# Kernel tuning notes

Measured on AMD Instinct MI355X. Metric: run time of the kernel, lower is better.

Reference implementation:

```python
import jax, jax.numpy as jnp
import numpy as np

_D4H = (np.array([
    0,0,0,0, -4,0,0,0, -2,-2,-2,-2, -2,-2,-2,0, -2,-2,-2,2, -2,-2,0,-2, -2,-2,0,0, -2,-2,0,2,
    -2,-2,2,-2, -2,-2,2,0, -2,-2,2,2, -2,0,-2,-2, -2,0,-2,0, -2,0,-2,2, -2,0,0,-2, -2,0,0,0,
    -2,0,0,2, -2,0,2,-2, -2,0,2,0, -2,0,2,2, -2,2,-2,-2, -2,2,-2,0, -2,2,-2,2, -2,2,0,-2,
    -2,2,0,0, -2,2,0,2, -2,2,2,-2, -2,2,2,0, -2,2,2,2, 0,-4,0,0, 0,-2,-2,-2, 0,-2,-2,0,
    0,-2,-2,2, 0,-2,0,-2, 0,-2,0,0, 0,-2,0,2, 0,-2,2,-2, 0,-2,2,0, 0,-2,2,2, 0,0,-4,0,
    0,0,-2,-2, 0,0,-2,0, 0,0,-2,2, 0,0,0,-4, 0,0,0,-2,
    -3,-1,-3,-1, -3,-1,-3,1, -3,-1,-1,-3, -3,-1,-1,-1, -3,-1,-1,1, -3,-1,-1,3, -3,-1,1,-3, -3,-1,1,-1,
    -3,-1,1,1, -3,-1,1,3, -3,-1,3,-1, -3,-1,3,1, -3,1,-3,-1, -3,1,-3,1, -3,1,-1,-3, -3,1,-1,-1,
    -3,1,-1,1, -3,1,-1,3, -3,1,1,-3, -3,1,1,-1, -3,1,1,1, -3,1,1,3, -3,1,3,-1, -3,1,3,1,
    -3,3,-1,-1, -3,3,1,-1, -3,3,1,1, -1,-3,-3,-1, -1,-3,-3,1, -1,-3,-1,-3, -1,-3,-1,-1, -1,-3,-1,1,
    -1,-3,-1,3, -1,-3,1,-3, -1,-3,1,-1, -1,-3,1,1, -1,-3,1,3, -1,-3,3,-1, -1,-3,3,1, -1,-1,-3,-3,
    -1,-1,-3,-1, -1,-1,-3,1, -1,-1,-3,3, -1,-1,-1,-3, -1,-1,-1,-1, -1,-1,-1,1, -1,-1,-1,3, -1,-1,1,-3,
    -1,-1,1,-1, -1,-1,1,1, -1,-1,1,3, -1,-1,3,-3, -1,-1,3,-1, -1,-1,3,1, -1,-1,3,3, -1,1,-3,-3,
    -1,1,-3,-1, -1,1,-3,1, -1,1,-3,3, -1,1,-1,-3, -1,1,-1,-1, -1,1,-1,1, -1,1,-1,3, -1,1,1,-3,
    -1,1,1,-1, -1,1,1,1, -1,1,1,3, -1,1,3,-3, -1,1,3,-1, -1,1,3,1, -1,1,3,3, -1,3,-3,-1,
    -1,3,-3,1, -1,3,-1,-3, -1,3,-1,-1, -1,3,-1,1, -1,3,-1,3, -1,3,1,-3, -1,3,1,-1, -1,3,1,1,
    -1,3,1,3, -1,3,3,-1, -1,3,3,1
], dtype=np.float32).reshape(128, 4) / 2.0)

M_OUT = 4096   # out_features (q1*q2)
IN_F = 4096    # in_features (p1*p2)
NGRP = IN_F // 4
BATCH = 256

def setup_inputs():
    key = jax.random.key(0)
    k1, k2, k3, k4 = jax.random.split(key, 4)
    return {
        "input": jax.random.normal(k1, (BATCH, IN_F), jnp.float32),
        "scaleW_DSC": jax.random.uniform(k2, (IN_F,), jnp.float32, 0.5, 1.5),
        "Qscales": jax.random.uniform(k3, (NGRP,), jnp.float32, 0.5, 1.5),
        "Qidxs": jax.random.randint(k4, (M_OUT, NGRP), 0, 256, jnp.int32),
    }

def reference(input, scaleW_DSC, Qscales, Qidxs):
    D4H = jnp.asarray(_D4H)
    # incoherence / diagonal scaling of activations, then per-group-of-4 quant scales
    x = (input.reshape(-1, IN_F) * scaleW_DSC).reshape(-1, NGRP, 4)  # [b, n, 4]
    x = x * Qscales[None, :, None]
    # dequantize weights from the D4 half-codebook: top bit = sign, low 7 bits = row
    sign = jnp.where(Qidxs < 128, 1.0, -1.0).astype(x.dtype)         # [m, n]
    W = D4H[Qidxs & 127] * sign[:, :, None]                          # [m, n, 4]
    # z[b, i] = sum_j <x[b, j, :], W[i, j, :]>  (the indexsum8 gather-accumulate)
    z = jnp.einsum('bjk,ijk->bi', x, W)                              # [b, m]
    return z.reshape(*input.shape[:-1], M_OUT)
```

## Files before the change

kernel.cpp:

```cpp
#include <hip/hip_runtime.h>

#define DI __device__ __forceinline__

constexpr int BATCH = 256;
constexpr int INF   = 4096;
constexpr int NGRP  = 1024;
constexpr int MOUT  = 4096;

using bf16x8 = __attribute__((ext_vector_type(8))) short;
using f32x4  = __attribute__((ext_vector_type(4))) float;

__device__ __constant__ signed char D4_I8[512] = {
     0, 0, 0, 0,  -4, 0, 0, 0,  -2,-2,-2,-2,  -2,-2,-2, 0,  -2,-2,-2, 2,  -2,-2, 0,-2,  -2,-2, 0, 0,  -2,-2, 0, 2,
    -2,-2, 2,-2,  -2,-2, 2, 0,  -2,-2, 2, 2,  -2, 0,-2,-2,  -2, 0,-2, 0,  -2, 0,-2, 2,  -2, 0, 0,-2,  -2, 0, 0, 0,
    -2, 0, 0, 2,  -2, 0, 2,-2,  -2, 0, 2, 0,  -2, 0, 2, 2,  -2, 2,-2,-2,  -2, 2,-2, 0,  -2, 2,-2, 2,  -2, 2, 0,-2,
    -2, 2, 0, 0,  -2, 2, 0, 2,  -2, 2, 2,-2,  -2, 2, 2, 0,  -2, 2, 2, 2,   0,-4, 0, 0,   0,-2,-2,-2,   0,-2,-2, 0,
     0,-2,-2, 2,   0,-2, 0,-2,   0,-2, 0, 0,   0,-2, 0, 2,   0,-2, 2,-2,   0,-2, 2, 0,   0,-2, 2, 2,   0, 0,-4, 0,
     0, 0,-2,-2,   0, 0,-2, 0,   0, 0,-2, 2,   0, 0, 0,-4,   0, 0, 0,-2,
    -3,-1,-3,-1,  -3,-1,-3, 1,  -3,-1,-1,-3,  -3,-1,-1,-1,  -3,-1,-1, 1,  -3,-1,-1, 3,  -3,-1, 1,-3,  -3,-1, 1,-1,
    -3,-1, 1, 1,  -3,-1, 1, 3,  -3,-1, 3,-1,  -3,-1, 3, 1,  -3, 1,-3,-1,  -3, 1,-3, 1,  -3, 1,-1,-3,  -3, 1,-1,-1,
    -3, 1,-1, 1,  -3, 1,-1, 3,  -3, 1, 1,-3,  -3, 1, 1,-1,  -3, 1, 1, 1,  -3, 1, 1, 3,  -3, 1, 3,-1,  -3, 1, 3, 1,
    -3, 3,-1,-1,  -3, 3, 1,-1,  -3, 3, 1, 1,  -1,-3,-3,-1,  -1,-3,-3, 1,  -1,-3,-1,-3,  -1,-3,-1,-1,  -1,-3,-1, 1,
    -1,-3,-1, 3,  -1,-3, 1,-3,  -1,-3, 1,-1,  -1,-3, 1, 1,  -1,-3, 1, 3,  -1,-3, 3,-1,  -1,-3, 3, 1,  -1,-1,-3,-3,
    -1,-1,-3,-1,  -1,-1,-3, 1,  -1,-1,-3, 3,  -1,-1,-1,-3,  -1,-1,-1,-1,  -1,-1,-1, 1,  -1,-1,-1, 3,  -1,-1, 1,-3,
    -1,-1, 1,-1,  -1,-1, 1, 1,  -1,-1, 1, 3,  -1,-1, 3,-3,  -1,-1, 3,-1,  -1,-1, 3, 1,  -1,-1, 3, 3,  -1, 1,-3,-3,
    -1, 1,-3,-1,  -1, 1,-3, 1,  -1, 1,-3, 3,  -1, 1,-1,-3,  -1, 1,-1,-1,  -1, 1,-1, 1,  -1, 1,-1, 3,  -1, 1, 1,-3,
    -1, 1, 1,-1,  -1, 1, 1, 1,  -1, 1, 1, 3,  -1, 1, 3,-3,  -1, 1, 3,-1,  -1, 1, 3, 1,  -1, 1, 3, 3,  -1, 3,-3,-1,
    -1, 3,-3, 1,  -1, 3,-1,-3,  -1, 3,-1,-1,  -1, 3,-1, 1,  -1, 3,-1, 3,  -1, 3, 1,-3,  -1, 3, 1,-1,  -1, 3, 1, 1,
    -1, 3, 1, 3,  -1, 3, 3,-1,  -1, 3, 3, 1
};

DI unsigned short f2bf(float f) {
  unsigned int u = __float_as_uint(f);
  u += 0x7fffu + ((u >> 16) & 1u);
  return (unsigned short)(u >> 16);
}

__global__ __launch_bounds__(256) void prep_kernel(
    const float* __restrict__ inp, const float* __restrict__ sw,
    const float* __restrict__ qs, const int* __restrict__ qidx,
    unsigned short* __restrict__ xa, unsigned short* __restrict__ qp) {
  __shared__ unsigned short lw[16384];
  const int t = threadIdx.x;

  if (blockIdx.x < 512) {
    int i  = blockIdx.x * 256 + t;
    int j  = i & 3;
    int m  = (i >> 2) & 255;
    int kb = i >> 10;
    const float* ip = inp + (size_t)m * INF + kb * 32 + j * 8;
    float4 f0 = *reinterpret_cast<const float4*>(ip);
    float4 f1 = *reinterpret_cast<const float4*>(ip + 4);
    const float* sp = sw + kb * 32 + j * 8;
    float4 s0 = *reinterpret_cast<const float4*>(sp);
    float4 s1 = *reinterpret_cast<const float4*>(sp + 4);
    int g = kb * 8 + j * 2;
    float q0 = qs[g], q1 = qs[g + 1];
    union { unsigned short u[8]; uint4 v; } o;
    o.u[0] = f2bf(f0.x * s0.x * q0); o.u[1] = f2bf(f0.y * s0.y * q0);
    o.u[2] = f2bf(f0.z * s0.z * q0); o.u[3] = f2bf(f0.w * s0.w * q0);
    o.u[4] = f2bf(f1.x * s1.x * q1); o.u[5] = f2bf(f1.y * s1.y * q1);
    o.u[6] = f2bf(f1.z * s1.z * q1); o.u[7] = f2bf(f1.w * s1.w * q1);
    reinterpret_cast<uint4*>(xa)[i] = o.v;
    return;
  }

  const int n0 = (blockIdx.x - 512) * 32;
  char* lwb = reinterpret_cast<char*>(lw);
  const int b4w   = t >> 1;
  const int cbase = b4w * 256 + ((2 * t) & 3) * 2;
  const int xk    = (b4w & 31) << 3;
  for (int r = 0; r < 32; ++r) {
    int4 v = *reinterpret_cast<const int4*>(
        qidx + (size_t)(n0 + r) * NGRP + t * 4);
    unsigned p01 = (v.x & 255) | ((v.y & 255) << 8) |
                   ((v.z & 255) << 16) | ((unsigned)(v.w & 255) << 24);
    *reinterpret_cast<unsigned*>(lwb + cbase + ((r * 8) ^ xk)) = p01;
  }
  __syncthreads();
  for (int it = 0; it < 16; ++it) {
    int b4 = it * 8 + (t >> 5);
    int n  = t & 31;
    unsigned long long v = *reinterpret_cast<const unsigned long long*>(
        lwb + b4 * 256 + ((n * 8) ^ ((b4 & 31) << 3)));
    *reinterpret_cast<unsigned long long*>(
        reinterpret_cast<char*>(qp) + (size_t)b4 * 32768 +
        (size_t)(n0 + n) * 8) = v;
  }
}


#define MM(A, B, C) C = __builtin_amdgcn_mfma_f32_16x16x32_bf16(A, B, C, 0, 0, 0)
#define LD8(p) (*reinterpret_cast<const bf16x8*>(p))

#define BAR() do { \
    asm volatile("s_waitcnt lgkmcnt(0)\n\ts_barrier" ::: "memory"); \
    __builtin_amdgcn_sched_barrier(0); } while (0)

#define STG(QV, BUF) do { \
    ulonglong2 w_; \
    w_.x = tbl[(QV) & 255]; w_.y = tbl[(QV) >> 8]; \
    *reinterpret_cast<ulonglong2*>(wsm + wbase + (BUF) + wslot) = w_; } while (0)

#define AL(AB, T) do { \
    AB##_0 = LD8(axb + (size_t)(T) * 32768 +     0); \
    AB##_1 = LD8(axb + (size_t)(T) * 32768 +  1024); \
    AB##_2 = LD8(axb + (size_t)(T) * 32768 + 16384); \
    AB##_3 = LD8(axb + (size_t)(T) * 32768 + 17408); } while (0)

#define CMP(AB, BUFOFF) do { \
    const char* wp_ = wsm + kqW + (BUFOFF); \
    bf16x8 b00 = LD8(wp_ + rb00); \
    bf16x8 b01 = LD8(wp_ + rb00 + 2048); \
    bf16x8 b10 = LD8(wp_ + rb10); \
    bf16x8 b11 = LD8(wp_ + rb10 + 2048); \
    MM(AB##_0, b00, c00); MM(AB##_0, b01, c01); \
    MM(AB##_1, b00, c10); MM(AB##_1, b01, c11); \
    MM(AB##_2, b10, c00); MM(AB##_2, b11, c01); \
    MM(AB##_3, b10, c10); MM(AB##_3, b11, c11); } while (0)

#define STEPA(T, QN) do { \
    AL(AO, (T) + 1); STG(QN, (((T) + 1) & 1) * 4096); \
    CMP(AE, ((T) & 1) * 4096); BAR(); } while (0)
#define STEPB(T, QN) do { \
    AL(AE, (T) + 1); STG(QN, (((T) + 1) & 1) * 4096); \
    CMP(AO, ((T) & 1) * 4096); BAR(); } while (0)

__global__ __launch_bounds__(1024, 4) void gemm_kernel(
    const unsigned short* __restrict__ xa, const unsigned short* __restrict__ qp,
    float* __restrict__ out) {
  __shared__ unsigned long long tbl[256];
  __shared__ float red[12][1152];
  char* wsm = reinterpret_cast<char*>(red);

  const int tid  = threadIdx.x;
  const int lane = tid & 63;
  const int wave = tid >> 6;
  const int mh   = wave >> 2;
  const int kq   = wave & 3;
  const int l15  = lane & 15, l4 = lane >> 4;

  const int bid = blockIdx.x;
  const int ns  = bid & 127;
  const int mt  = bid >> 7;
  const int n0  = ns * 32;
  const int m0  = mt * 128 + mh * 32;

  const int kqs = tid >> 8;
  const int qn  = (tid & 255) >> 3;
  const int j2  = tid & 7;
  const unsigned wbase = (unsigned)(kqs * 8192);
  const unsigned wslot =
      ((unsigned)(qn * 128 + j2 * 16)) ^ ((unsigned)(qn & 7) << 4);

  const char* qpb = reinterpret_cast<const char*>(qp) +
      (size_t)(kqs * 32 + (j2 >> 2)) * 32768 + (size_t)(n0 + qn) * 8 +
      (j2 & 3) * 2;
#define QLD(K) ((unsigned)*reinterpret_cast<const unsigned short*>(qpb + (size_t)(K) * 65536))
  const unsigned Qs0 = QLD(0),  Qs1 = QLD(1),  Qs2 = QLD(2),  Qs3 = QLD(3);
  const unsigned Qs4 = QLD(4),  Qs5 = QLD(5),  Qs6 = QLD(6),  Qs7 = QLD(7);
  const unsigned Qs8 = QLD(8),  Qs9 = QLD(9),  Qsa = QLD(10), Qsb = QLD(11);
  const unsigned Qsc = QLD(12), Qsd = QLD(13), Qse = QLD(14), Qsf = QLD(15);
#undef QLD

  const char* axb = reinterpret_cast<const char*>(xa) +
      (size_t)(kq * 32) * 16384 + (size_t)(m0 + l15) * 64 + l4 * 16;
  const unsigned swzB = (unsigned)(l15 & 7) << 4;
  const unsigned kqW  = (unsigned)(kq * 8192);
  const unsigned rb00 = ((unsigned)(l15 * 128 + l4 * 16)) ^ swzB;
  const unsigned rb10 = ((unsigned)(l15 * 128 + 64 + l4 * 16)) ^ swzB;

  bf16x8 AE_0, AE_1, AE_2, AE_3, AO_0, AO_1, AO_2, AO_3;
  f32x4  c00 = {}, c01 = {}, c10 = {}, c11 = {};

  AL(AE, 0);

  if (tid < 256) {
    int r = tid & 127, sg = tid >> 7;
    unsigned long long v = 0;
#pragma unroll
    for (int j = 0; j < 4; ++j) {
      float f = (float)D4_I8[r * 4 + j] * 0.5f;
      unsigned int b = __float_as_uint(f) ^ (sg ? 0x80000000u : 0u);
      v |= (unsigned long long)(b >> 16) << (16 * j);
    }
    tbl[tid] = v;
  }
  BAR();
  STG(Qs0, 0);
  BAR();

  STEPA(0,  Qs1); STEPB(1,  Qs2); STEPA(2,  Qs3); STEPB(3,  Qs4);
  STEPA(4,  Qs5); STEPB(5,  Qs6); STEPA(6,  Qs7); STEPB(7,  Qs8);
  STEPA(8,  Qs9); STEPB(9,  Qsa); STEPA(10, Qsb); STEPB(11, Qsc);
  STEPA(12, Qsd); STEPB(13, Qse); STEPA(14, Qsf);
  CMP(AO, 4096);
  BAR();

#define PWR(C, MI, NI) do { \
    pl[((MI) * 16 + l4 * 4 + 0) * 36 + (NI) * 16 + l15] = C[0]; \
    pl[((MI) * 16 + l4 * 4 + 1) * 36 + (NI) * 16 + l15] = C[1]; \
    pl[((MI) * 16 + l4 * 4 + 2) * 36 + (NI) * 16 + l15] = C[2]; \
    pl[((MI) * 16 + l4 * 4 + 3) * 36 + (NI) * 16 + l15] = C[3]; } while (0)
#define PRD(C, MI, NI) do { \
    C[0] += pl[((MI) * 16 + l4 * 4 + 0) * 36 + (NI) * 16 + l15]; \
    C[1] += pl[((MI) * 16 + l4 * 4 + 1) * 36 + (NI) * 16 + l15]; \
    C[2] += pl[((MI) * 16 + l4 * 4 + 2) * 36 + (NI) * 16 + l15]; \
    C[3] += pl[((MI) * 16 + l4 * 4 + 3) * 36 + (NI) * 16 + l15]; } while (0)

  if (kq) {
    float* pl = &red[mh * 3 + kq - 1][0];
    PWR(c00, 0, 0); PWR(c01, 0, 1); PWR(c10, 1, 0); PWR(c11, 1, 1);
  }
  __syncthreads();
  if (kq == 0) {
#pragma unroll
    for (int p = 0; p < 3; ++p) {
      const float* pl = &red[mh * 3 + p][0];
      PRD(c00, 0, 0); PRD(c01, 0, 1); PRD(c10, 1, 0); PRD(c11, 1, 1);
    }
    float* ob = out + (size_t)(m0 + l4 * 4) * MOUT + n0 + l15;
#define STO(C, MI, NI) do { \
    ob[(size_t)((MI) * 16 + 0) * MOUT + (NI) * 16] = C[0]; \
    ob[(size_t)((MI) * 16 + 1) * MOUT + (NI) * 16] = C[1]; \
    ob[(size_t)((MI) * 16 + 2) * MOUT + (NI) * 16] = C[2]; \
    ob[(size_t)((MI) * 16 + 3) * MOUT + (NI) * 16] = C[3]; } while (0)
    STO(c00, 0, 0); STO(c01, 0, 1); STO(c10, 1, 0); STO(c11, 1, 1);
#undef STO
  }
#undef PWR
#undef PRD
}

extern "C" void kernel_launch(void* const* d_in, const int* in_sizes, int n_in,
                              void* d_out, int out_size, void* d_ws, size_t ws_size,
                              hipStream_t stream) {
  const float* inp = (const float*)d_in[0];
  const float* sw  = (const float*)d_in[1];
  const float* qs  = (const float*)d_in[2];
  const int*   qi  = (const int*)d_in[3];
  float* out = (float*)d_out;
  unsigned short* xa = (unsigned short*)d_ws;
  unsigned short* qp = (unsigned short*)((char*)d_ws + (4 << 20));

  prep_kernel<<<640, 256, 0, stream>>>(inp, sw, qs, qi, xa, qp);
  gemm_kernel<<<256, 1024, 0, stream>>>(xa, qp, out);
}
```

Baseline: 29.62 us.

## Retile GEMM waves to 2x8 split-K with 64-row tiles and tree reduction

```diff
diff --git a/kernel.cpp b/kernel.cpp
--- a/kernel.cpp
+++ b/kernel.cpp
@@ -103,60 +103,57 @@
     *reinterpret_cast<ulonglong2*>(wsm + wbase + (BUF) + wslot) = w_; } while (0)
 
 #define AL(AB, T) do { \
-    AB##_0 = LD8(axb + (size_t)(T) * 32768 +     0); \
-    AB##_1 = LD8(axb + (size_t)(T) * 32768 +  1024); \
-    AB##_2 = LD8(axb + (size_t)(T) * 32768 + 16384); \
-    AB##_3 = LD8(axb + (size_t)(T) * 32768 + 17408); } while (0)
+    AB##_0 = LD8(axb + (size_t)(T) * 16384 +    0); \
+    AB##_1 = LD8(axb + (size_t)(T) * 16384 + 1024); \
+    AB##_2 = LD8(axb + (size_t)(T) * 16384 + 2048); \
+    AB##_3 = LD8(axb + (size_t)(T) * 16384 + 3072); } while (0)
 
 #define CMP(AB, BUFOFF) do { \
     const char* wp_ = wsm + kqW + (BUFOFF); \
-    bf16x8 b00 = LD8(wp_ + rb00); \
-    bf16x8 b01 = LD8(wp_ + rb00 + 2048); \
-    bf16x8 b10 = LD8(wp_ + rb10); \
-    bf16x8 b11 = LD8(wp_ + rb10 + 2048); \
-    MM(AB##_0, b00, c00); MM(AB##_0, b01, c01); \
-    MM(AB##_1, b00, c10); MM(AB##_1, b01, c11); \
-    MM(AB##_2, b10, c00); MM(AB##_2, b11, c01); \
-    MM(AB##_3, b10, c10); MM(AB##_3, b11, c11); } while (0)
+    bf16x8 b0 = LD8(wp_ + rb0); \
+    bf16x8 b1 = LD8(wp_ + rb1); \
+    MM(AB##_0, b0, c00); MM(AB##_0, b1, c01); \
+    MM(AB##_1, b0, c10); MM(AB##_1, b1, c11); \
+    MM(AB##_2, b0, c20); MM(AB##_2, b1, c21); \
+    MM(AB##_3, b0, c30); MM(AB##_3, b1, c31); } while (0)
 
 #define STEPA(T, QN) do { \
-    AL(AO, (T) + 1); STG(QN, (((T) + 1) & 1) * 4096); \
-    CMP(AE, ((T) & 1) * 4096); BAR(); } while (0)
+    AL(AO, (T) + 1); STG(QN, (((T) + 1) & 1) * 2048); \
+    CMP(AE, ((T) & 1) * 2048); BAR(); } while (0)
 #define STEPB(T, QN) do { \
-    AL(AE, (T) + 1); STG(QN, (((T) + 1) & 1) * 4096); \
-    CMP(AO, ((T) & 1) * 4096); BAR(); } while (0)
+    AL(AE, (T) + 1); STG(QN, (((T) + 1) & 1) * 2048); \
+    CMP(AO, ((T) & 1) * 2048); BAR(); } while (0)
 
 __global__ __launch_bounds__(1024, 4) void gemm_kernel(
     const unsigned short* __restrict__ xa, const unsigned short* __restrict__ qp,
     float* __restrict__ out) {
-  __shared__ unsigned long long tbl[256];
-  __shared__ float red[12][1152];
-  char* wsm = reinterpret_cast<char*>(red);
+  __shared__ float red[8][64 * 36];
+  unsigned long long* tbl =
+      reinterpret_cast<unsigned long long*>(&red[0][0]);
+  char* wsm = reinterpret_cast<char*>(&red[0][0]) + 2048;
 
   const int tid  = threadIdx.x;
   const int lane = tid & 63;
   const int wave = tid >> 6;
-  const int mh   = wave >> 2;
-  const int kq   = wave & 3;
+  const int mh   = wave >> 3;
+  const int kq   = wave & 7;
   const int l15  = lane & 15, l4 = lane >> 4;
 
   const int bid = blockIdx.x;
   const int ns  = bid & 127;
   const int mt  = bid >> 7;
   const int n0  = ns * 32;
-  const int m0  = mt * 128 + mh * 32;
-
-  const int kqs = tid >> 8;
-  const int qn  = (tid & 255) >> 3;
-  const int j2  = tid & 7;
-  const unsigned wbase = (unsigned)(kqs * 8192);
-  const unsigned wslot =
-      ((unsigned)(qn * 128 + j2 * 16)) ^ ((unsigned)(qn & 7) << 4);
+  const int m0  = mt * 128 + mh * 64;
+
+  const int kqs = tid >> 7;
+  const int qn  = tid & 31;
+  const int j2  = (tid >> 5) & 3;
+  const unsigned wbase = (unsigned)(kqs * 4096);
+  const unsigned wslot = (unsigned)(j2 * 512 + qn * 16);
 
   const char* qpb = reinterpret_cast<const char*>(qp) +
-      (size_t)(kqs * 32 + (j2 >> 2)) * 32768 + (size_t)(n0 + qn) * 8 +
-      (j2 & 3) * 2;
-#define QLD(K) ((unsigned)*reinterpret_cast<const unsigned short*>(qpb + (size_t)(K) * 65536))
+      (size_t)(kqs * 16) * 32768 + (size_t)(n0 + qn) * 8 + j2 * 2;
+#define QLD(K) ((unsigned)*reinterpret_cast<const unsigned short*>(qpb + (size_t)(K) * 32768))
   const unsigned Qs0 = QLD(0),  Qs1 = QLD(1),  Qs2 = QLD(2),  Qs3 = QLD(3);
   const unsigned Qs4 = QLD(4),  Qs5 = QLD(5),  Qs6 = QLD(6),  Qs7 = QLD(7);
   const unsigned Qs8 = QLD(8),  Qs9 = QLD(9),  Qsa = QLD(10), Qsb = QLD(11);
@@ -164,14 +161,14 @@
 #undef QLD
 
   const char* axb = reinterpret_cast<const char*>(xa) +
-      (size_t)(kq * 32) * 16384 + (size_t)(m0 + l15) * 64 + l4 * 16;
-  const unsigned swzB = (unsigned)(l15 & 7) << 4;
-  const unsigned kqW  = (unsigned)(kq * 8192);
-  const unsigned rb00 = ((unsigned)(l15 * 128 + l4 * 16)) ^ swzB;
-  const unsigned rb10 = ((unsigned)(l15 * 128 + 64 + l4 * 16)) ^ swzB;
+      (size_t)(kq * 16) * 16384 + (size_t)(m0 + l15) * 64 + l4 * 16;
+  const unsigned kqW = (unsigned)(kq * 4096);
+  const unsigned rb0 = (unsigned)(l4 * 512 + l15 * 16);
+  const unsigned rb1 = rb0 + 256;
 
   bf16x8 AE_0, AE_1, AE_2, AE_3, AO_0, AO_1, AO_2, AO_3;
   f32x4  c00 = {}, c01 = {}, c10 = {}, c11 = {};
+  f32x4  c20 = {}, c21 = {}, c30 = {}, c31 = {};
 
   AL(AE, 0);
 
@@ -194,31 +191,38 @@
   STEPA(4,  Qs5); STEPB(5,  Qs6); STEPA(6,  Qs7); STEPB(7,  Qs8);
   STEPA(8,  Qs9); STEPB(9,  Qsa); STEPA(10, Qsb); STEPB(11, Qsc);
   STEPA(12, Qsd); STEPB(13, Qse); STEPA(14, Qsf);
-  CMP(AO, 4096);
-  BAR();
-
-#define PWR(C, MI, NI) do { \
+  CMP(AO, 2048);
+  BAR();
+
+#define PWR(PL) do { float* pl = (PL); \
+    PW1(c00, 0, 0); PW1(c01, 0, 1); PW1(c10, 1, 0); PW1(c11, 1, 1); \
+    PW1(c20, 2, 0); PW1(c21, 2, 1); PW1(c30, 3, 0); PW1(c31, 3, 1); } while (0)
+#define PW1(C, MI, NI) do { \
     pl[((MI) * 16 + l4 * 4 + 0) * 36 + (NI) * 16 + l15] = C[0]; \
     pl[((MI) * 16 + l4 * 4 + 1) * 36 + (NI) * 16 + l15] = C[1]; \
     pl[((MI) * 16 + l4 * 4 + 2) * 36 + (NI) * 16 + l15] = C[2]; \
     pl[((MI) * 16 + l4 * 4 + 3) * 36 + (NI) * 16 + l15] = C[3]; } while (0)
-#define PRD(C, MI, NI) do { \
+#define PRD(PL) do { const float* pl = (PL); \
+    PR1(c00, 0, 0); PR1(c01, 0, 1); PR1(c10, 1, 0); PR1(c11, 1, 1); \
+    PR1(c20, 2, 0); PR1(c21, 2, 1); PR1(c30, 3, 0); PR1(c31, 3, 1); } while (0)
+#define PR1(C, MI, NI) do { \
     C[0] += pl[((MI) * 16 + l4 * 4 + 0) * 36 + (NI) * 16 + l15]; \
     C[1] += pl[((MI) * 16 + l4 * 4 + 1) * 36 + (NI) * 16 + l15]; \
     C[2] += pl[((MI) * 16 + l4 * 4 + 2) * 36 + (NI) * 16 + l15]; \
     C[3] += pl[((MI) * 16 + l4 * 4 + 3) * 36 + (NI) * 16 + l15]; } while (0)
 
-  if (kq) {
-    float* pl = &red[mh * 3 + kq - 1][0];
-    PWR(c00, 0, 0); PWR(c01, 0, 1); PWR(c10, 1, 0); PWR(c11, 1, 1);
-  }
-  __syncthreads();
+  if (kq >= 4) PWR(&red[mh * 4 + kq - 4][0]);
+  BAR();
+  if (kq < 4)  PRD(&red[mh * 4 + kq][0]);
+  BAR();
+  if (kq == 2 || kq == 3) PWR(&red[mh * 4 + kq - 2][0]);
+  BAR();
+  if (kq < 2)  PRD(&red[mh * 4 + kq][0]);
+  BAR();
+  if (kq == 1) PWR(&red[mh * 4][0]);
+  BAR();
   if (kq == 0) {
-#pragma unroll
-    for (int p = 0; p < 3; ++p) {
-      const float* pl = &red[mh * 3 + p][0];
-      PRD(c00, 0, 0); PRD(c01, 0, 1); PRD(c10, 1, 0); PRD(c11, 1, 1);
-    }
+    PRD(&red[mh * 4][0]);
     float* ob = out + (size_t)(m0 + l4 * 4) * MOUT + n0 + l15;
 #define STO(C, MI, NI) do { \
     ob[(size_t)((MI) * 16 + 0) * MOUT + (NI) * 16] = C[0]; \
@@ -226,10 +230,13 @@
     ob[(size_t)((MI) * 16 + 2) * MOUT + (NI) * 16] = C[2]; \
     ob[(size_t)((MI) * 16 + 3) * MOUT + (NI) * 16] = C[3]; } while (0)
     STO(c00, 0, 0); STO(c01, 0, 1); STO(c10, 1, 0); STO(c11, 1, 1);
+    STO(c20, 2, 0); STO(c21, 2, 1); STO(c30, 3, 0); STO(c31, 3, 1);
 #undef STO
   }
 #undef PWR
+#undef PW1
 #undef PRD
+#undef PR1
 }
 
 extern "C" void kernel_launch(void* const* d_in, const int* in_sizes, int n_in,
```

After: 31.14 us. 5.1% more time.

## Double K-step depth per pipeline stage to halve barrier count

Applied to the files above, without the earlier changes.

```diff
diff --git a/kernel.cpp b/kernel.cpp
--- a/kernel.cpp
+++ b/kernel.cpp
@@ -97,41 +97,58 @@
     asm volatile("s_waitcnt lgkmcnt(0)\n\ts_barrier" ::: "memory"); \
     __builtin_amdgcn_sched_barrier(0); } while (0)
 
-#define STG(QV, BUF) do { \
+#define STG2(QLO, QHI, BUF) do { \
     ulonglong2 w_; \
-    w_.x = tbl[(QV) & 255]; w_.y = tbl[(QV) >> 8]; \
-    *reinterpret_cast<ulonglong2*>(wsm + wbase + (BUF) + wslot) = w_; } while (0)
+    w_.x = tbl[(QLO) & 255]; w_.y = tbl[(QLO) >> 8]; \
+    *reinterpret_cast<ulonglong2*>(wsm + wbase + (BUF) + wslot) = w_; \
+    w_.x = tbl[(QHI) & 255]; w_.y = tbl[(QHI) >> 8]; \
+    *reinterpret_cast<ulonglong2*>(wsm + wbase + (BUF) + wslot + 128) = w_; } while (0)
 
 #define AL(AB, T) do { \
-    AB##_0 = LD8(axb + (size_t)(T) * 32768 +     0); \
-    AB##_1 = LD8(axb + (size_t)(T) * 32768 +  1024); \
-    AB##_2 = LD8(axb + (size_t)(T) * 32768 + 16384); \
-    AB##_3 = LD8(axb + (size_t)(T) * 32768 + 17408); } while (0)
-
-#define CMP(AB, BUFOFF) do { \
-    const char* wp_ = wsm + kqW + (BUFOFF); \
-    bf16x8 b00 = LD8(wp_ + rb00); \
-    bf16x8 b01 = LD8(wp_ + rb00 + 2048); \
-    bf16x8 b10 = LD8(wp_ + rb10); \
-    bf16x8 b11 = LD8(wp_ + rb10 + 2048); \
+    const char* ax_ = axb + (size_t)(T) * 65536; \
+    AB##_0 = LD8(ax_ +     0); AB##_1 = LD8(ax_ +  1024); \
+    AB##_2 = LD8(ax_ + 16384); AB##_3 = LD8(ax_ + 17408); \
+    AB##_4 = LD8(ax_ + 32768); AB##_5 = LD8(ax_ + 33792); \
+    AB##_6 = LD8(ax_ + 49152); AB##_7 = LD8(ax_ + 50176); } while (0)
+
+#define MFMA16(AB, b00,b01,b10,b11,b20,b21,b30,b31) do { \
     MM(AB##_0, b00, c00); MM(AB##_0, b01, c01); \
     MM(AB##_1, b00, c10); MM(AB##_1, b01, c11); \
     MM(AB##_2, b10, c00); MM(AB##_2, b11, c01); \
-    MM(AB##_3, b10, c10); MM(AB##_3, b11, c11); } while (0)
-
-#define STEPA(T, QN) do { \
-    AL(AO, (T) + 1); STG(QN, (((T) + 1) & 1) * 4096); \
-    CMP(AE, ((T) & 1) * 4096); BAR(); } while (0)
-#define STEPB(T, QN) do { \
-    AL(AE, (T) + 1); STG(QN, (((T) + 1) & 1) * 4096); \
-    CMP(AO, ((T) & 1) * 4096); BAR(); } while (0)
+    MM(AB##_3, b10, c10); MM(AB##_3, b11, c11); \
+    MM(AB##_4, b20, c00); MM(AB##_4, b21, c01); \
+    MM(AB##_5, b20, c10); MM(AB##_5, b21, c11); \
+    MM(AB##_6, b30, c00); MM(AB##_6, b31, c01); \
+    MM(AB##_7, b30, c10); MM(AB##_7, b31, c11); } while (0)
+
+#define BREADS() \
+    bf16x8 b00 = LD8(wp_ + rk0), b01 = LD8(wp_ + rk0 + 4096); \
+    bf16x8 b10 = LD8(wp_ + rk1), b11 = LD8(wp_ + rk1 + 4096); \
+    bf16x8 b20 = LD8(wp_ + rk2), b21 = LD8(wp_ + rk2 + 4096); \
+    bf16x8 b30 = LD8(wp_ + rk3), b31 = LD8(wp_ + rk3 + 4096);
+
+#define STEPA(T, QLO, QHI) do { \
+    const char* wp_ = wsm + kqW + ((T) & 1) * 8192; \
+    BREADS() \
+    STG2(QLO, QHI, (((T) + 1) & 1) * 8192); \
+    AL(AO, (T) + 1); \
+    MFMA16(AE, b00,b01,b10,b11,b20,b21,b30,b31); \
+    BAR(); } while (0)
+#define STEPB(T, QLO, QHI) do { \
+    const char* wp_ = wsm + kqW + ((T) & 1) * 8192; \
+    BREADS() \
+    STG2(QLO, QHI, (((T) + 1) & 1) * 8192); \
+    AL(AE, (T) + 1); \
+    MFMA16(AO, b00,b01,b10,b11,b20,b21,b30,b31); \
+    BAR(); } while (0)
 
 __global__ __launch_bounds__(1024, 4) void gemm_kernel(
     const unsigned short* __restrict__ xa, const unsigned short* __restrict__ qp,
     float* __restrict__ out) {
   __shared__ unsigned long long tbl[256];
-  __shared__ float red[12][1152];
-  char* wsm = reinterpret_cast<char*>(red);
+  __shared__ ulonglong2 wt[4096];
+  char*  wsm  = reinterpret_cast<char*>(wt);
+  float* redp = reinterpret_cast<float*>(wt);
 
   const int tid  = threadIdx.x;
   const int lane = tid & 63;
@@ -149,28 +166,36 @@
   const int kqs = tid >> 8;
   const int qn  = (tid & 255) >> 3;
   const int j2  = tid & 7;
-  const unsigned wbase = (unsigned)(kqs * 8192);
+  const unsigned wbase = (unsigned)(kqs * 16384);
   const unsigned wslot =
-      ((unsigned)(qn * 128 + j2 * 16)) ^ ((unsigned)(qn & 7) << 4);
+      ((unsigned)(qn * 256 + j2 * 16)) ^ ((unsigned)(qn & 7) << 4);
 
   const char* qpb = reinterpret_cast<const char*>(qp) +
       (size_t)(kqs * 32 + (j2 >> 2)) * 32768 + (size_t)(n0 + qn) * 8 +
       (j2 & 3) * 2;
-#define QLD(K) ((unsigned)*reinterpret_cast<const unsigned short*>(qpb + (size_t)(K) * 65536))
-  const unsigned Qs0 = QLD(0),  Qs1 = QLD(1),  Qs2 = QLD(2),  Qs3 = QLD(3);
-  const unsigned Qs4 = QLD(4),  Qs5 = QLD(5),  Qs6 = QLD(6),  Qs7 = QLD(7);
-  const unsigned Qs8 = QLD(8),  Qs9 = QLD(9),  Qsa = QLD(10), Qsb = QLD(11);
-  const unsigned Qsc = QLD(12), Qsd = QLD(13), Qse = QLD(14), Qsf = QLD(15);
-#undef QLD
+#define QLDB(OFF) ((unsigned)*reinterpret_cast<const unsigned short*>(qpb + (OFF)))
+  const unsigned QA0 = QLDB(0),       QB0 = QLDB(65536);
+  const unsigned QA1 = QLDB(131072),  QB1 = QLDB(196608);
+  const unsigned QA2 = QLDB(262144),  QB2 = QLDB(327680);
+  const unsigned QA3 = QLDB(393216),  QB3 = QLDB(458752);
+  const unsigned QA4 = QLDB(524288),  QB4 = QLDB(589824);
+  const unsigned QA5 = QLDB(655360),  QB5 = QLDB(720896);
+  const unsigned QA6 = QLDB(786432),  QB6 = QLDB(851968);
+  const unsigned QA7 = QLDB(917504),  QB7 = QLDB(983040);
+#undef QLDB
 
   const char* axb = reinterpret_cast<const char*>(xa) +
-      (size_t)(kq * 32) * 16384 + (size_t)(m0 + l15) * 64 + l4 * 16;
+      (size_t)kq * 524288 + (size_t)(m0 + l15) * 64 + l4 * 16;
+  const unsigned kqW  = (unsigned)(kq * 16384);
   const unsigned swzB = (unsigned)(l15 & 7) << 4;
-  const unsigned kqW  = (unsigned)(kq * 8192);
-  const unsigned rb00 = ((unsigned)(l15 * 128 + l4 * 16)) ^ swzB;
-  const unsigned rb10 = ((unsigned)(l15 * 128 + 64 + l4 * 16)) ^ swzB;
-
-  bf16x8 AE_0, AE_1, AE_2, AE_3, AO_0, AO_1, AO_2, AO_3;
+  const unsigned rbB  = (unsigned)(l15 * 256 + l4 * 16);
+  const unsigned rk0 = (rbB +   0) ^ swzB;
+  const unsigned rk1 = (rbB +  64) ^ swzB;
+  const unsigned rk2 = (rbB + 128) ^ swzB;
+  const unsigned rk3 = (rbB + 192) ^ swzB;
+
+  bf16x8 AE_0, AE_1, AE_2, AE_3, AE_4, AE_5, AE_6, AE_7;
+  bf16x8 AO_0, AO_1, AO_2, AO_3, AO_4, AO_5, AO_6, AO_7;
   f32x4  c00 = {}, c01 = {}, c10 = {}, c11 = {};
 
   AL(AE, 0);
@@ -187,14 +212,18 @@
     tbl[tid] = v;
   }
   BAR();
-  STG(Qs0, 0);
+  STG2(QA0, QB0, 0);
   BAR();
 
-  STEPA(0,  Qs1); STEPB(1,  Qs2); STEPA(2,  Qs3); STEPB(3,  Qs4);
-  STEPA(4,  Qs5); STEPB(5,  Qs6); STEPA(6,  Qs7); STEPB(7,  Qs8);
-  STEPA(8,  Qs9); STEPB(9,  Qsa); STEPA(10, Qsb); STEPB(11, Qsc);
-  STEPA(12, Qsd); STEPB(13, Qse); STEPA(14, Qsf);
-  CMP(AO, 4096);
+  STEPA(0, QA1, QB1); STEPB(1, QA2, QB2);
+  STEPA(2, QA3, QB3); STEPB(3, QA4, QB4);
+  STEPA(4, QA5, QB5); STEPB(5, QA6, QB6);
+  STEPA(6, QA7, QB7);
+  {
+    const char* wp_ = wsm + kqW + 8192;
+    BREADS()
+    MFMA16(AO, b00,b01,b10,b11,b20,b21,b30,b31);
+  }
   BAR();
 
 #define PWR(C, MI, NI) do { \
@@ -209,14 +238,14 @@
     C[3] += pl[((MI) * 16 + l4 * 4 + 3) * 36 + (NI) * 16 + l15]; } while (0)
 
   if (kq) {
-    float* pl = &red[mh * 3 + kq - 1][0];
+    float* pl = redp + (size_t)(mh * 3 + kq - 1) * 1152;
     PWR(c00, 0, 0); PWR(c01, 0, 1); PWR(c10, 1, 0); PWR(c11, 1, 1);
   }
   __syncthreads();
   if (kq == 0) {
 #pragma unroll
     for (int p = 0; p < 3; ++p) {
-      const float* pl = &red[mh * 3 + p][0];
+      const float* pl = redp + (size_t)(mh * 3 + p) * 1152;
       PRD(c00, 0, 0); PRD(c01, 0, 1); PRD(c10, 1, 0); PRD(c11, 1, 1);
     }
     float* ob = out + (size_t)(m0 + l4 * 4) * MOUT + n0 + l15;
```

New measurement: 29.48 us. Within noise of the previous version (-0.5%).
